# Kernel tuning notes

Hardware: AMD Instinct MI355X
Metric: run time of the kernel (lower is better)

## Reference

```python
import jax, jax.numpy as jnp
import numpy as np


def setup_inputs() -> dict:
    key = jax.random.key(0)
    k1, k2 = jax.random.split(key)
    B, H, V, N = 256, 4096, 1024, 32
    v = jax.random.uniform(k1, (B, V, N), dtype=jnp.float32)
    W = jax.random.normal(k2, (H, V, N), dtype=jnp.float32) / np.sqrt(V * N + 2)
    b_h = jnp.zeros((H,), dtype=jnp.float32)
    b_v = jnp.zeros((V, N), dtype=jnp.float32)
    return {"v": v, "W": W, "b_h": b_h, "b_v": b_v}


def reference(v, W, b_h, b_v):
    # (v.unsqueeze(-3) * W).sum([-1,-2]) is a contraction over (visible, category):
    # einsum 'bvn,hvn->bh' — a GEMM with K = n_visible * n.
    logits = jnp.einsum('bvn,hvn->bh', v, W) + b_h          # [B, H]
    sp = jax.nn.softplus(logits).sum(-1)                     # [B]
    vt = jnp.einsum('bvn,vn->b', v, b_v)                     # [B]
    return sp + vt
```

## Files before the change

### kernel.cpp

```cpp
#include <hip/hip_runtime.h>
#include <hip/hip_bf16.h>
#include <stdint.h>

#define B_ 256
#define H_ 4096
#define K_ 32768

typedef __attribute__((ext_vector_type(8))) short bf16x8;
typedef __attribute__((ext_vector_type(4))) float f32x4;

__device__ __forceinline__ unsigned short f2bf(float x) {
    union { float f; unsigned int u; } c; c.f = x;
    unsigned int r = c.u + 0x7FFFu + ((c.u >> 16) & 1u);
    return (unsigned short)(r >> 16);
}

__device__ __forceinline__ short bfc(float x) {
    __hip_bfloat16 h = __float2bfloat16(x);
    union { __hip_bfloat16 h; short s; } c; c.h = h;
    return c.s;
}

__device__ __forceinline__ float softplus_f(float x) {
    return fmaxf(x, 0.0f) + log1pf(expf(-fabsf(x)));
}

__global__ __launch_bounds__(256) void prep_kernel(
    const float* __restrict__ v, const float* __restrict__ bv,
    __hip_bfloat16* __restrict__ vbf, float* __restrict__ vt)
{
    const int b = blockIdx.x;
    const int t = threadIdx.x;
    const float* vr = v + (size_t)b * K_;
    unsigned short* dr = (unsigned short*)(vbf + (size_t)b * K_);
    float acc = 0.f;
    for (int i = t * 8; i < K_; i += 256 * 8) {
        float4 x0 = *(const float4*)(vr + i);
        float4 x1 = *(const float4*)(vr + i + 4);
        float4 b0 = *(const float4*)(bv + i);
        float4 b1 = *(const float4*)(bv + i + 4);
        acc += x0.x*b0.x + x0.y*b0.y + x0.z*b0.z + x0.w*b0.w
             + x1.x*b1.x + x1.y*b1.y + x1.z*b1.z + x1.w*b1.w;
        ushort4 u0, u1;
        u0.x = f2bf(x0.x); u0.y = f2bf(x0.y); u0.z = f2bf(x0.z); u0.w = f2bf(x0.w);
        u1.x = f2bf(x1.x); u1.y = f2bf(x1.y); u1.z = f2bf(x1.z); u1.w = f2bf(x1.w);
        *(ushort4*)(dr + i)     = u0;
        *(ushort4*)(dr + i + 4) = u1;
    }
    __shared__ float sm[256];
    sm[t] = acc;
    __syncthreads();
    for (int s = 128; s > 0; s >>= 1) {
        if (t < s) sm[t] += sm[t + s];
        __syncthreads();
    }
    if (t == 0) vt[b] = sm[0];
}


#define NCONS 8

#define LOAD_AS(S_, kt) do {                                                           \
    aC[(S_)]     = *(const bf16x8*)(ap[0] + (size_t)(kt) * 64 + (S_) * 32);            \
    aC[2 + (S_)] = *(const bf16x8*)(ap[1] + (size_t)(kt) * 64 + (S_) * 32);            \
    } while (0)

#define COMPUTE_S(T_, S_) do {                                                         \
    const unsigned short* wb_ = &wtile[(T_) & 3][0];                                   \
    _Pragma("unroll")                                                                  \
    for (int q_ = 0; q_ < 2; ++q_) {                                                   \
        bf16x8 bfr[4];                                                                 \
        _Pragma("unroll")                                                              \
        for (int n_ = 0; n_ < 4; ++n_) {                                               \
            int row_ = (q_ * 4 + n_) * 16 + lr;                                        \
            bfr[n_] = *(const bf16x8*)&wb_[row_ * 64 +                                 \
                        ((((S_) * 4 + lg) ^ (row_ & 7)) << 3)];                        \
        }                                                                              \
        _Pragma("unroll")                                                              \
        for (int m_ = 0; m_ < 2; ++m_)                                                 \
            _Pragma("unroll")                                                          \
            for (int n_ = 0; n_ < 4; ++n_)                                             \
                acc[m_][q_ * 4 + n_] = __builtin_amdgcn_mfma_f32_16x16x32_bf16(        \
                    aC[m_ * 2 + (S_)], bfr[n_], acc[m_][q_ * 4 + n_], 0, 0, 0);        \
    } } while (0)

#define PISS(dst, HIDX) do {                                                           \
    _Pragma("unroll")                                                                  \
    for (int j_ = 0; j_ < 4; ++j_) {                                                   \
        const float* p_ = prow[j_] + (size_t)((HIDX) & 1) * 64 * K_                    \
                                   + (size_t)((HIDX) >> 1) * 64;                       \
        dst[2*j_]   = *(const float4*)p_;                                              \
        dst[2*j_+1] = *(const float4*)(p_ + 4);                                        \
    } } while (0)

#define PWRITE(src, T_, HALF_) do {                                                    \
    _Pragma("unroll")                                                                  \
    for (int j_ = 0; j_ < 4; ++j_) {                                                   \
        int R_ = (HALF_) * 64 + j_ * 16 + pw * 8 + r8;                                 \
        float4 a_ = src[2*j_], b_ = src[2*j_+1];                                       \
        bf16x8 u_;                                                                     \
        u_[0]=bfc(a_.x); u_[1]=bfc(a_.y); u_[2]=bfc(a_.z); u_[3]=bfc(a_.w);            \
        u_[4]=bfc(b_.x); u_[5]=bfc(b_.y); u_[6]=bfc(b_.z); u_[7]=bfc(b_.w);            \
        *(bf16x8*)&wtile[(T_) & 3][R_ * 64 + swz] = u_;                                \
    } } while (0)

#define VMW(N)  asm volatile("s_waitcnt vmcnt(" #N ")" ::: "memory")
#define PBAR()  asm volatile("s_waitcnt lgkmcnt(0)\n\ts_barrier" ::: "memory")
#define CBAR()  asm volatile("s_barrier" ::: "memory")

__global__ __launch_bounds__(640, 4) void gemm_kernel(
    const __hip_bfloat16* __restrict__ vbf,
    const float* __restrict__ W,
    float* __restrict__ part,
    int KS, int NT)
{
    __shared__ __align__(16) unsigned short wtile[4][128 * 64];

    const int tid  = threadIdx.x;
    const int wid  = tid >> 6;
    const int lane = tid & 63;
    const int lr   = lane & 15;
    const int lg   = lane >> 4;

    const int bid   = blockIdx.x;
    const int sidx  = bid % KS;
    const int ht    = bid / KS;
    const int h0    = ht * 128;
    const int kbase = sidx * (NT * 64);

    if (wid < NCONS) {
        const __hip_bfloat16* ap[2];
        #pragma unroll
        for (int m = 0; m < 2; ++m)
            ap[m] = vbf + (size_t)(wid * 32 + m * 16 + lr) * K_ + kbase + lg * 8;

        f32x4 acc[2][8];
        #pragma unroll
        for (int m = 0; m < 2; ++m)
            #pragma unroll
            for (int n = 0; n < 8; ++n)
                acc[m][n] = (f32x4)(0.0f);

        bf16x8 aC[4];
        LOAD_AS(0, 0);
        LOAD_AS(1, 0);
        CBAR();

        for (int t = 0; t < NT; ++t) {
            const bool last = (t == NT - 1);
            COMPUTE_S(t, 0);
            if (!last) LOAD_AS(0, t + 1);
            COMPUTE_S(t, 1);
            if (!last) LOAD_AS(1, t + 1);
            CBAR();
        }

        float* pout = part + (size_t)sidx * ((size_t)B_ * H_) + h0;
        #pragma unroll
        for (int m = 0; m < 2; ++m)
            #pragma unroll
            for (int n = 0; n < 8; ++n)
                #pragma unroll
                for (int j = 0; j < 4; ++j) {
                    int brow = wid * 32 + m * 16 + lg * 4 + j;
                    int hcol = n * 16 + lr;
                    pout[(size_t)brow * H_ + hcol] = acc[m][n][j];
                }
    } else {
        const int pw = wid - NCONS;
        const int l8 = lane & 7;
        const int r8 = lane >> 3;
        const float* prow[4];
        #pragma unroll
        for (int j = 0; j < 4; ++j)
            prow[j] = W + (size_t)(h0 + j * 16 + pw * 8 + r8) * K_ + kbase + l8 * 8;
        const int swz = ((l8 ^ r8) << 3);

        float4 bufA[8], bufB[8];

        PISS(bufA, 0);
        PISS(bufB, 1);
        VMW(8);  PWRITE(bufA, 0, 0);  PISS(bufA, 2);
        VMW(8);  PWRITE(bufB, 0, 1);  PISS(bufB, 3);
        PBAR();

        for (int t = 0; t < NT - 1; ++t) {
            const bool lastp = (t == NT - 2);
            VMW(8);
            PWRITE(bufA, t + 1, 0);
            if (!lastp) PISS(bufA, 2 * (t + 2));
            if (lastp) { VMW(0); } else { VMW(8); }
            PWRITE(bufB, t + 1, 1);
            if (!lastp) PISS(bufB, 2 * (t + 2) + 1);
            PBAR();
        }
        PBAR();
    }
}

__global__ __launch_bounds__(256) void reduce_kernel(
    const float* __restrict__ part, const float* __restrict__ bh,
    const float* __restrict__ vt, float* __restrict__ out, int KS)
{
    const int b = blockIdx.x;
    const int t = threadIdx.x;
    float sp = 0.f;
    const float* pb = part + (size_t)b * H_;
    for (int h = t * 4; h < H_; h += 256 * 4) {
        float4 l = *(const float4*)(bh + h);
        for (int s = 0; s < KS; ++s) {
            float4 p = *(const float4*)(pb + (size_t)s * B_ * H_ + h);
            l.x += p.x; l.y += p.y; l.z += p.z; l.w += p.w;
        }
        sp += softplus_f(l.x) + softplus_f(l.y) + softplus_f(l.z) + softplus_f(l.w);
    }
    __shared__ float sm[256];
    sm[t] = sp;
    __syncthreads();
    for (int r = 128; r > 0; r >>= 1) {
        if (t < r) sm[t] += sm[t + r];
        __syncthreads();
    }
    if (t == 0) out[b] = sm[0] + vt[b];
}

extern "C" void kernel_launch(void* const* d_in, const int* in_sizes, int n_in,
                              void* d_out, int out_size, void* d_ws, size_t ws_size,
                              hipStream_t stream)
{
    const float* v  = (const float*)d_in[0];
    const float* W  = (const float*)d_in[1];
    const float* bh = (const float*)d_in[2];
    const float* bv = (const float*)d_in[3];
    float* out = (float*)d_out;

    char* ws = (char*)d_ws;
    const size_t vbf_bytes = (size_t)B_ * K_ * sizeof(__hip_bfloat16);
    __hip_bfloat16* vbf = (__hip_bfloat16*)ws;

    int KS = 16;
    while (KS > 1 && vbf_bytes + (size_t)KS * B_ * H_ * 4 + 1024 > ws_size) KS >>= 1;

    float* part = (float*)(ws + vbf_bytes);
    float* vt   = (float*)(ws + vbf_bytes + (size_t)KS * B_ * H_ * 4);

    prep_kernel<<<B_, 256, 0, stream>>>(v, bv, vbf, vt);
    const int NT = (K_ / KS) / 64;
    gemm_kernel<<<(H_ / 128) * KS, 640, 0, stream>>>(vbf, W, part, KS, NT);
    reduce_kernel<<<B_, 256, 0, stream>>>(part, bh, vt, out, KS);
}
```

Baseline: 197.3 us.

## Widen K tile to 256 with double-buffered LDS and finer-grained producer pipeline

Enlarges the per-iteration K tile from 64 to 256, switching the W staging tile from four 64-wide slots to two 256-wide slots (128 KB LDS), which cuts the barrier count by four. The producer waves now stream W in 32 chunks per tile, cycling through four small register buffers with a vmcnt-based software pipeline. The consumer waves load A fragments directly in the inner loop rather than prefetching them a tile ahead. Fewer barriers and finer-grained load overlap are the goal, but the 128 KB of LDS per block may cut occupancy below the declared launch bounds, and A loads are no longer hidden behind the previous tile's compute.

```diff
diff --git a/kernel.cpp b/kernel.cpp
--- a/kernel.cpp
+++ b/kernel.cpp
@@ -59,54 +59,25 @@
 
 
 #define NCONS 8
-
-#define LOAD_AS(S_, kt) do {                                                           \
-    aC[(S_)]     = *(const bf16x8*)(ap[0] + (size_t)(kt) * 64 + (S_) * 32);            \
-    aC[2 + (S_)] = *(const bf16x8*)(ap[1] + (size_t)(kt) * 64 + (S_) * 32);            \
-    } while (0)
-
-#define COMPUTE_S(T_, S_) do {                                                         \
-    const unsigned short* wb_ = &wtile[(T_) & 3][0];                                   \
-    _Pragma("unroll")                                                                  \
-    for (int q_ = 0; q_ < 2; ++q_) {                                                   \
-        bf16x8 bfr[4];                                                                 \
-        _Pragma("unroll")                                                              \
-        for (int n_ = 0; n_ < 4; ++n_) {                                               \
-            int row_ = (q_ * 4 + n_) * 16 + lr;                                        \
-            bfr[n_] = *(const bf16x8*)&wb_[row_ * 64 +                                 \
-                        ((((S_) * 4 + lg) ^ (row_ & 7)) << 3)];                        \
-        }                                                                              \
-        _Pragma("unroll")                                                              \
-        for (int m_ = 0; m_ < 2; ++m_)                                                 \
-            _Pragma("unroll")                                                          \
-            for (int n_ = 0; n_ < 4; ++n_)                                             \
-                acc[m_][q_ * 4 + n_] = __builtin_amdgcn_mfma_f32_16x16x32_bf16(        \
-                    aC[m_ * 2 + (S_)], bfr[n_], acc[m_][q_ * 4 + n_], 0, 0, 0);        \
-    } } while (0)
-
-#define PISS(dst, HIDX) do {                                                           \
-    _Pragma("unroll")                                                                  \
-    for (int j_ = 0; j_ < 4; ++j_) {                                                   \
-        const float* p_ = prow[j_] + (size_t)((HIDX) & 1) * 64 * K_                    \
-                                   + (size_t)((HIDX) >> 1) * 64;                       \
-        dst[2*j_]   = *(const float4*)p_;                                              \
-        dst[2*j_+1] = *(const float4*)(p_ + 4);                                        \
-    } } while (0)
-
-#define PWRITE(src, T_, HALF_) do {                                                    \
-    _Pragma("unroll")                                                                  \
-    for (int j_ = 0; j_ < 4; ++j_) {                                                   \
-        int R_ = (HALF_) * 64 + j_ * 16 + pw * 8 + r8;                                 \
-        float4 a_ = src[2*j_], b_ = src[2*j_+1];                                       \
-        bf16x8 u_;                                                                     \
-        u_[0]=bfc(a_.x); u_[1]=bfc(a_.y); u_[2]=bfc(a_.z); u_[3]=bfc(a_.w);            \
-        u_[4]=bfc(b_.x); u_[5]=bfc(b_.y); u_[6]=bfc(b_.z); u_[7]=bfc(b_.w);            \
-        *(bf16x8*)&wtile[(T_) & 3][R_ * 64 + swz] = u_;                                \
-    } } while (0)
-
 #define VMW(N)  asm volatile("s_waitcnt vmcnt(" #N ")" ::: "memory")
 #define PBAR()  asm volatile("s_waitcnt lgkmcnt(0)\n\ts_barrier" ::: "memory")
 #define CBAR()  asm volatile("s_barrier" ::: "memory")
+
+#define P_ISS(BUF, TT, CC) do {                                                        \
+    const float* p_ = wlb + (size_t)((CC) >> 2) * (16 * (size_t)K_)                    \
+                          + (size_t)(TT) * 256 + ((CC) & 3) * 64;                      \
+    BUF[0] = *(const float4*)p_;                                                       \
+    BUF[1] = *(const float4*)(p_ + 4);                                                 \
+    } while (0)
+
+#define P_WR(BUF, SLOT_, CC) do {                                                      \
+    int r_ = (((CC) >> 2) & 7) * 16 + rsub;                                            \
+    int g_ = ((((CC) & 3) * 8 + l8) ^ r7);                                             \
+    bf16x8 u_;                                                                         \
+    u_[0]=bfc(BUF[0].x); u_[1]=bfc(BUF[0].y); u_[2]=bfc(BUF[0].z); u_[3]=bfc(BUF[0].w);\
+    u_[4]=bfc(BUF[1].x); u_[5]=bfc(BUF[1].y); u_[6]=bfc(BUF[1].z); u_[7]=bfc(BUF[1].w);\
+    *(bf16x8*)&wtile[(SLOT_) + r_ * 256 + g_ * 8] = u_;                                \
+    } while (0)
 
 __global__ __launch_bounds__(640, 4) void gemm_kernel(
     const __hip_bfloat16* __restrict__ vbf,
@@ -114,7 +85,7 @@
     float* __restrict__ part,
     int KS, int NT)
 {
-    __shared__ __align__(16) unsigned short wtile[4][128 * 64];
+    __shared__ __align__(16) unsigned short wtile[2 * 128 * 256];
 
     const int tid  = threadIdx.x;
     const int wid  = tid >> 6;
@@ -126,13 +97,11 @@
     const int sidx  = bid % KS;
     const int ht    = bid / KS;
     const int h0    = ht * 128;
-    const int kbase = sidx * (NT * 64);
+    const int kbase = sidx * (NT * 256);
 
     if (wid < NCONS) {
-        const __hip_bfloat16* ap[2];
-        #pragma unroll
-        for (int m = 0; m < 2; ++m)
-            ap[m] = vbf + (size_t)(wid * 32 + m * 16 + lr) * K_ + kbase + lg * 8;
+        const __hip_bfloat16* ap0 = vbf + (size_t)(wid * 32 + lr) * K_ + kbase + lg * 8;
+        const __hip_bfloat16* ap1 = ap0 + (size_t)16 * K_;
 
         f32x4 acc[2][8];
         #pragma unroll
@@ -141,17 +110,33 @@
             for (int n = 0; n < 8; ++n)
                 acc[m][n] = (f32x4)(0.0f);
 
-        bf16x8 aC[4];
-        LOAD_AS(0, 0);
-        LOAD_AS(1, 0);
         CBAR();
 
         for (int t = 0; t < NT; ++t) {
-            const bool last = (t == NT - 1);
-            COMPUTE_S(t, 0);
-            if (!last) LOAD_AS(0, t + 1);
-            COMPUTE_S(t, 1);
-            if (!last) LOAD_AS(1, t + 1);
+            const unsigned short* wb = &wtile[(t & 1) * 32768];
+            const size_t koff = (size_t)t * 256;
+            #pragma unroll
+            for (int s = 0; s < 8; ++s) {
+                bf16x8 a0 = *(const bf16x8*)(ap0 + koff + s * 32);
+                bf16x8 a1 = *(const bf16x8*)(ap1 + koff + s * 32);
+                #pragma unroll
+                for (int q = 0; q < 2; ++q) {
+                    bf16x8 bfr[4];
+                    #pragma unroll
+                    for (int n = 0; n < 4; ++n) {
+                        int row = (q * 4 + n) * 16 + lr;
+                        int g   = (s * 4 + lg) ^ (lr & 7);
+                        bfr[n] = *(const bf16x8*)&wb[row * 256 + g * 8];
+                    }
+                    #pragma unroll
+                    for (int n = 0; n < 4; ++n) {
+                        acc[0][q*4+n] = __builtin_amdgcn_mfma_f32_16x16x32_bf16(
+                            a0, bfr[n], acc[0][q*4+n], 0, 0, 0);
+                        acc[1][q*4+n] = __builtin_amdgcn_mfma_f32_16x16x32_bf16(
+                            a1, bfr[n], acc[1][q*4+n], 0, 0, 0);
+                    }
+                }
+            }
             CBAR();
         }
 
@@ -167,31 +152,53 @@
                     pout[(size_t)brow * H_ + hcol] = acc[m][n][j];
                 }
     } else {
-        const int pw = wid - NCONS;
-        const int l8 = lane & 7;
-        const int r8 = lane >> 3;
-        const float* prow[4];
+        const int gl   = (wid - NCONS) * 64 + lane;
+        const int rsub = gl >> 3;
+        const int l8   = gl & 7;
+        const int r7   = rsub & 7;
+        const float* wlb = W + (size_t)(h0 + rsub) * K_ + kbase + l8 * 8;
+
+        float4 buf0[2], buf1[2], buf2[2], buf3[2];
+
+        P_ISS(buf0, 0, 0); P_ISS(buf1, 0, 1); P_ISS(buf2, 0, 2); P_ISS(buf3, 0, 3);
+
         #pragma unroll
-        for (int j = 0; j < 4; ++j)
-            prow[j] = W + (size_t)(h0 + j * 16 + pw * 8 + r8) * K_ + kbase + l8 * 8;
-        const int swz = ((l8 ^ r8) << 3);
-
-        float4 bufA[8], bufB[8];
-
-        PISS(bufA, 0);
-        PISS(bufB, 1);
-        VMW(8);  PWRITE(bufA, 0, 0);  PISS(bufA, 2);
-        VMW(8);  PWRITE(bufB, 0, 1);  PISS(bufB, 3);
+        for (int c = 0; c < 32; ++c) {
+            VMW(6);
+            if ((c & 3) == 0) { P_WR(buf0, 0, c); if (c < 28) P_ISS(buf0, 0, c+4); else P_ISS(buf0, 1, c-28); }
+            if ((c & 3) == 1) { P_WR(buf1, 0, c); if (c < 28) P_ISS(buf1, 0, c+4); else P_ISS(buf1, 1, c-28); }
+            if ((c & 3) == 2) { P_WR(buf2, 0, c); if (c < 28) P_ISS(buf2, 0, c+4); else P_ISS(buf2, 1, c-28); }
+            if ((c & 3) == 3) { P_WR(buf3, 0, c); if (c < 28) P_ISS(buf3, 0, c+4); else P_ISS(buf3, 1, c-28); }
+        }
         PBAR();
 
-        for (int t = 0; t < NT - 1; ++t) {
-            const bool lastp = (t == NT - 2);
-            VMW(8);
-            PWRITE(bufA, t + 1, 0);
-            if (!lastp) PISS(bufA, 2 * (t + 2));
-            if (lastp) { VMW(0); } else { VMW(8); }
-            PWRITE(bufB, t + 1, 1);
-            if (!lastp) PISS(bufB, 2 * (t + 2) + 1);
+        for (int t = 0; t < NT - 2; ++t) {
+            const int slot = ((t + 1) & 1) * 32768;
+            #pragma unroll
+            for (int c = 0; c < 32; ++c) {
+                VMW(6);
+                if ((c & 3) == 0) { P_WR(buf0, slot, c); if (c < 28) P_ISS(buf0, t+1, c+4); else P_ISS(buf0, t+2, c-28); }
+                if ((c & 3) == 1) { P_WR(buf1, slot, c); if (c < 28) P_ISS(buf1, t+1, c+4); else P_ISS(buf1, t+2, c-28); }
+                if ((c & 3) == 2) { P_WR(buf2, slot, c); if (c < 28) P_ISS(buf2, t+1, c+4); else P_ISS(buf2, t+2, c-28); }
+                if ((c & 3) == 3) { P_WR(buf3, slot, c); if (c < 28) P_ISS(buf3, t+1, c+4); else P_ISS(buf3, t+2, c-28); }
+            }
+            PBAR();
+        }
+
+        {
+            const int slot = ((NT - 1) & 1) * 32768;
+            #pragma unroll
+            for (int c = 0; c < 28; ++c) {
+                VMW(6);
+                if ((c & 3) == 0) { P_WR(buf0, slot, c); P_ISS(buf0, NT-1, c+4); }
+                if ((c & 3) == 1) { P_WR(buf1, slot, c); P_ISS(buf1, NT-1, c+4); }
+                if ((c & 3) == 2) { P_WR(buf2, slot, c); P_ISS(buf2, NT-1, c+4); }
+                if ((c & 3) == 3) { P_WR(buf3, slot, c); P_ISS(buf3, NT-1, c+4); }
+            }
+            VMW(6); P_WR(buf0, slot, 28);
+            VMW(4); P_WR(buf1, slot, 29);
+            VMW(2); P_WR(buf2, slot, 30);
+            VMW(0); P_WR(buf3, slot, 31);
             PBAR();
         }
         PBAR();
@@ -245,7 +252,7 @@
     float* vt   = (float*)(ws + vbf_bytes + (size_t)KS * B_ * H_ * 4);
 
     prep_kernel<<<B_, 256, 0, stream>>>(v, bv, vbf, vt);
-    const int NT = (K_ / KS) / 64;
+    const int NT = (K_ / KS) / 256;
     gemm_kernel<<<(H_ / 128) * KS, 640, 0, stream>>>(vbf, W, part, KS, NT);
     reduce_kernel<<<B_, 256, 0, stream>>>(part, bh, vt, out, KS);
 }
```

Result: slower. 221.1 us (+12.1%).
